# Kernel tuning notes

Measured on AMD Instinct MI355X. Metric: run time of the kernel, lower is better.

The kernel has to match this reference:

```python
import jax, jax.numpy as jnp
import numpy as np

B, N, F, D, H = 4, 2048, 128, 128, 4

def setup_inputs() -> dict:
    key = jax.random.key(0)
    k1, k2, k3, k4 = jax.random.split(key, 4)
    X = jax.random.normal(k1, (B, N, F), dtype=jnp.float32)
    A = jax.random.uniform(k2, (B, N, N), dtype=jnp.float32)
    kernel = jax.random.normal(k3, (F, D), dtype=jnp.float32) * 0.05
    bias = jnp.ones((D,), dtype=jnp.float32)
    attn = jax.random.normal(k4, (H, D, D), dtype=jnp.float32) * 0.05
    return {"X": X, "A": A, "kernel": kernel, "bias": bias, "attn": attn}

def reference(X, A, kernel, bias, attn):
    # Linear projection: [B,N,F] @ [F,D] + bias -> [B,N,D]
    Xp = jnp.einsum('bnf,fd->bnd', X, kernel) + bias
    # Per-head bilinear scores Xp @ attn_h @ Xp^T, batched over heads: [B,H,N,N]
    scores = jnp.einsum('bnd,hde,bme->bhnm', Xp, attn, Xp)
    # Adjacency mask + tanh (fused elementwise)
    Am = jnp.tanh(A[:, None, :, :] * scores)
    # Weighted aggregate per head: [B,H,N,N] @ [B,N,D] -> [B,H,N,D]
    heads = jnp.einsum('bhnm,bmd->bhnd', Am, Xp)
    # Mean over heads, relu
    Xh = jax.nn.relu(jnp.mean(heads, axis=1))
    # Skip connection (shapes match since F == D): relu(Xh + X)
    out = jax.nn.relu(Xh + X)
    return out
```

## Files before the change

### kernel.cpp

```cpp
#include <hip/hip_runtime.h>

#define NB 4
#define NN 2048
#define ND 128
#define NH 4

typedef short short8 __attribute__((ext_vector_type(8)));
typedef short short4v __attribute__((ext_vector_type(4)));
typedef float floatx4 __attribute__((ext_vector_type(4)));

__device__ __forceinline__ short f2bf(float f){
  unsigned u = __float_as_uint(f);
  u += 0x7FFFu + ((u >> 16) & 1u);
  return (short)(u >> 16);
}
__device__ __forceinline__ float bf2f(short s){
  unsigned u = ((unsigned)(unsigned short)s) << 16;
  return __uint_as_float(u);
}

__global__ void k0_transpose(const float* __restrict__ W, const float* __restrict__ attn,
                             short* __restrict__ WT, short* __restrict__ attnT){
  int mat = blockIdx.x;
  const float* src = (mat == 0) ? W : (attn + (mat - 1) * 16384);
  short* dst = (mat == 0) ? WT : (attnT + (mat - 1) * 16384);
  __shared__ short tile[128 * 130];
  int t = threadIdx.x;
  for (int k = 0; k < 64; ++k){
    int idx = k * 256 + t;
    int r = idx >> 7, c = idx & 127;
    tile[c * 130 + r] = f2bf(src[idx]);
  }
  __syncthreads();
  for (int k = 0; k < 8; ++k){
    int g = k * 256 + t;
    int r = g >> 4, c8 = g & 15;
    short8 v;
    #pragma unroll
    for (int j = 0; j < 8; ++j) v[j] = tile[r * 130 + c8 * 8 + j];
    *(short8*)&dst[r * 128 + c8 * 8] = v;
  }
}

__global__ __launch_bounds__(256) void k1_xp(const float* __restrict__ X,
                                             const short* __restrict__ WT,
                                             const float* __restrict__ bias,
                                             short* __restrict__ Xp){
  int bid = blockIdx.x;
  int b = bid >> 5, i0 = (bid & 31) << 6;
  int t = threadIdx.x, w = t >> 6, lane = t & 63, lq = lane >> 4, lc = lane & 15;
  __shared__ __align__(16) short ldsB[16384];
  #pragma unroll
  for (int c = 0; c < 8; ++c){
    int q = c * 256 + t; int fblk = q >> 7; int d = q & 127;
    *(short8*)&ldsB[q * 8] = *(const short8*)&WT[d * 128 + fblk * 8];
  }
  short8 af[4][4];
  #pragma unroll
  for (int ib = 0; ib < 4; ++ib)
    #pragma unroll
    for (int k = 0; k < 4; ++k){
      const float* xp = &X[(b * NN + i0 + ib * 16 + lc) * ND + k * 32 + lq * 8];
      float4 x0 = *(const float4*)xp;
      float4 x1 = *(const float4*)(xp + 4);
      short8 s;
      s[0]=f2bf(x0.x); s[1]=f2bf(x0.y); s[2]=f2bf(x0.z); s[3]=f2bf(x0.w);
      s[4]=f2bf(x1.x); s[5]=f2bf(x1.y); s[6]=f2bf(x1.z); s[7]=f2bf(x1.w);
      af[ib][k] = s;
    }
  __syncthreads();
  floatx4 acc[4][2];
  #pragma unroll
  for (int ib = 0; ib < 4; ++ib)
    #pragma unroll
    for (int eb = 0; eb < 2; ++eb) acc[ib][eb] = (floatx4){0.f, 0.f, 0.f, 0.f};
  #pragma unroll
  for (int eb = 0; eb < 2; ++eb)
    #pragma unroll
    for (int k = 0; k < 4; ++k){
      short8 bf = *(short8*)&ldsB[(k * 4 + lq) * 1024 + (w * 32 + eb * 16 + lc) * 8];
      #pragma unroll
      for (int ib = 0; ib < 4; ++ib)
        acc[ib][eb] = __builtin_amdgcn_mfma_f32_16x16x32_bf16(af[ib][k], bf, acc[ib][eb], 0, 0, 0);
    }
  #pragma unroll
  for (int ib = 0; ib < 4; ++ib)
    #pragma unroll
    for (int eb = 0; eb < 2; ++eb){
      int d = w * 32 + eb * 16 + lc;
      float bv = bias[d];
      #pragma unroll
      for (int r = 0; r < 4; ++r){
        int n = i0 + ib * 16 + lq * 4 + r;
        Xp[(b * NN + n) * ND + d] = f2bf(acc[ib][eb][r] + bv);
      }
    }
}

__global__ void k1b_transpose(const short* __restrict__ Xp, short* __restrict__ XpT){
  int bid = blockIdx.x;
  int b = bid >> 6; int rem = bid & 63;
  int n0 = (rem >> 1) << 6, d0 = (rem & 1) << 6;
  __shared__ short tile[64 * 66];
  int t = threadIdx.x;
  #pragma unroll
  for (int c = 0; c < 2; ++c){
    int g = c * 256 + t; int r = g >> 3, c8 = g & 7;
    short8 v = *(const short8*)&Xp[(b * NN + n0 + r) * ND + d0 + c8 * 8];
    #pragma unroll
    for (int j = 0; j < 8; ++j) tile[(c8 * 8 + j) * 66 + r] = v[j];
  }
  __syncthreads();
  #pragma unroll
  for (int c = 0; c < 2; ++c){
    int g = c * 256 + t; int d = g >> 3, n8 = g & 7;
    short8 v;
    #pragma unroll
    for (int j = 0; j < 8; ++j) v[j] = tile[d * 66 + n8 * 8 + j];
    *(short8*)&XpT[(b * ND + d0 + d) * NN + n0 + n8 * 8] = v;
  }
}

__global__ __launch_bounds__(256) void k2_y(const short* __restrict__ Xp,
                                            const short* __restrict__ attnT,
                                            short* __restrict__ Y){
  int bid = blockIdx.x;
  int it = bid & 31, h = (bid >> 5) & 3, b = bid >> 7;
  int i0 = it << 6;
  int t = threadIdx.x, w = t >> 6, lane = t & 63, lq = lane >> 4, lc = lane & 15;
  __shared__ __align__(16) short ldsB[16384];
  const short* Bsrc = attnT + h * 16384;
  #pragma unroll
  for (int c = 0; c < 8; ++c){
    int q = c * 256 + t; int dblk = q >> 7; int e = q & 127;
    *(short8*)&ldsB[q * 8] = *(const short8*)&Bsrc[e * 128 + dblk * 8];
  }
  short8 af[4][4];
  #pragma unroll
  for (int ib = 0; ib < 4; ++ib)
    #pragma unroll
    for (int k = 0; k < 4; ++k)
      af[ib][k] = *(const short8*)&Xp[(b * NN + i0 + ib * 16 + lc) * ND + k * 32 + lq * 8];
  __syncthreads();
  floatx4 acc[4][2];
  #pragma unroll
  for (int ib = 0; ib < 4; ++ib)
    #pragma unroll
    for (int eb = 0; eb < 2; ++eb) acc[ib][eb] = (floatx4){0.f, 0.f, 0.f, 0.f};
  #pragma unroll
  for (int eb = 0; eb < 2; ++eb)
    #pragma unroll
    for (int k = 0; k < 4; ++k){
      short8 bf = *(short8*)&ldsB[(k * 4 + lq) * 1024 + (w * 32 + eb * 16 + lc) * 8];
      #pragma unroll
      for (int ib = 0; ib < 4; ++ib)
        acc[ib][eb] = __builtin_amdgcn_mfma_f32_16x16x32_bf16(af[ib][k], bf, acc[ib][eb], 0, 0, 0);
    }
  #pragma unroll
  for (int ib = 0; ib < 4; ++ib)
    #pragma unroll
    for (int eb = 0; eb < 2; ++eb){
      int e = w * 32 + eb * 16 + lc;
      #pragma unroll
      for (int r = 0; r < 4; ++r){
        int n = i0 + ib * 16 + lq * 4 + r;
        Y[((b * NH + h) * NN + n) * ND + e] = f2bf(acc[ib][eb][r]);
      }
    }
}

__global__ __launch_bounds__(256, 3) void k3_fused(const short* __restrict__ Xp,
                                                   const short* __restrict__ XpT,
                                                   const short* __restrict__ Y,
                                                   const float* __restrict__ A,
                                                   float* __restrict__ part){
  int bid = blockIdx.x;
  int it = bid & 127, b = (bid >> 7) & 3, ms = bid >> 9;
  int i0 = it << 4;
  int t = threadIdx.x, w = t >> 6, lane = t & 63, lq = lane >> 4, lc = lane & 15;

  __shared__ __align__(16) short ldsXpT[2][8320];
  __shared__ __align__(16) short ldsPh[2][1024];
  __shared__ __align__(16) short ldsPl[2][1024];

  short8 yf[4][4];
  #pragma unroll
  for (int h = 0; h < 4; ++h)
    #pragma unroll
    for (int k = 0; k < 4; ++k)
      yf[h][k] = *(const short8*)&Y[((b * NH + h) * NN + i0 + lc) * ND + k * 32 + lq * 8];

  floatx4 acc[2];
  acc[0] = (floatx4){0.f,0.f,0.f,0.f};
  acc[1] = (floatx4){0.f,0.f,0.f,0.f};

  const int mbase = ms << 9;
  const int poff = (w * 2 + (lq >> 1)) * 128 + lc * 8 + (lq & 1) * 4;

  for (int itn = 0; itn < 8; ++itn){
    int p = itn & 1;
    int m0 = mbase + itn * 64;
    const short* src = XpT + b * (ND * NN) + m0;
    #pragma unroll
    for (int c = 0; c < 4; ++c){
      int q = c * 256 + t; int d = q >> 3, mb = q & 7;
      *(short8*)&ldsXpT[p][mb * 1040 + d * 8] = *(const short8*)&src[d * NN + mb * 8];
    }
    short8 xpf[4];
    const short* xr = Xp + (b * NN + m0 + w * 16 + lc) * ND;
    #pragma unroll
    for (int k = 0; k < 4; ++k) xpf[k] = *(const short8*)&xr[k * 32 + lq * 8];
    floatx4 av = *(const floatx4*)&A[(b * NN + i0 + lc) * NN + m0 + w * 16 + lq * 4];

    float psum[4] = {0.f, 0.f, 0.f, 0.f};
    #pragma unroll
    for (int h = 0; h < 4; ++h){
      floatx4 S = (floatx4){0.f,0.f,0.f,0.f};
      #pragma unroll
      for (int k = 0; k < 4; ++k)
        S = __builtin_amdgcn_mfma_f32_16x16x32_bf16(xpf[k], yf[h][k], S, 0, 0, 0);
      #pragma unroll
      for (int r = 0; r < 4; ++r){
        float x = av[r] * S[r];
        float e = __builtin_amdgcn_exp2f(x * 2.885390081777926f);
        psum[r] += 1.f - 2.f * __builtin_amdgcn_rcpf(e + 1.f);
      }
    }
    short4v hi4, lo4;
    #pragma unroll
    for (int r = 0; r < 4; ++r){
      float pb = 0.25f * psum[r];
      short h16 = f2bf(pb);
      hi4[r] = h16;
      lo4[r] = f2bf(pb - bf2f(h16));
    }
    *(short4v*)&ldsPh[p][poff] = hi4;
    *(short4v*)&ldsPl[p][poff] = lo4;
    __syncthreads();

    #pragma unroll
    for (int kb = 0; kb < 2; ++kb){
      short8 ph = *(short8*)&ldsPh[p][(kb * 4 + lq) * 128 + lc * 8];
      short8 pl = *(short8*)&ldsPl[p][(kb * 4 + lq) * 128 + lc * 8];
      #pragma unroll
      for (int db = 0; db < 2; ++db){
        short8 bfr = *(short8*)&ldsXpT[p][(kb * 4 + lq) * 1040 + (w * 32 + db * 16 + lc) * 8];
        acc[db] = __builtin_amdgcn_mfma_f32_16x16x32_bf16(ph, bfr, acc[db], 0, 0, 0);
        acc[db] = __builtin_amdgcn_mfma_f32_16x16x32_bf16(pl, bfr, acc[db], 0, 0, 0);
      }
    }
  }
  float* dst = part + (size_t)ms * 1048576 + (b * NN + i0) * ND;
  #pragma unroll
  for (int db = 0; db < 2; ++db)
    #pragma unroll
    for (int r = 0; r < 4; ++r)
      dst[(lq * 4 + r) * ND + w * 32 + db * 16 + lc] = acc[db][r];
}

__global__ void k4_final(const float* __restrict__ part, const float* __restrict__ X,
                         float* __restrict__ out){
  int f = (blockIdx.x * 256 + threadIdx.x) * 4;
  float4 s0 = *(const float4*)(part + f);
  float4 s1 = *(const float4*)(part + 1048576 + f);
  float4 s2 = *(const float4*)(part + 2097152 + f);
  float4 s3 = *(const float4*)(part + 3145728 + f);
  float4 xv = *(const float4*)(X + f);
  float4 o;
  o.x = fmaxf(fmaxf(s0.x + s1.x + s2.x + s3.x, 0.f) + xv.x, 0.f);
  o.y = fmaxf(fmaxf(s0.y + s1.y + s2.y + s3.y, 0.f) + xv.y, 0.f);
  o.z = fmaxf(fmaxf(s0.z + s1.z + s2.z + s3.z, 0.f) + xv.z, 0.f);
  o.w = fmaxf(fmaxf(s0.w + s1.w + s2.w + s3.w, 0.f) + xv.w, 0.f);
  *(float4*)(out + f) = o;
}

extern "C" void kernel_launch(void* const* d_in, const int* in_sizes, int n_in,
                              void* d_out, int out_size, void* d_ws, size_t ws_size,
                              hipStream_t stream) {
  const float* X    = (const float*)d_in[0];
  const float* A    = (const float*)d_in[1];
  const float* W    = (const float*)d_in[2];
  const float* bias = (const float*)d_in[3];
  const float* attn = (const float*)d_in[4];
  float* out = (float*)d_out;

  const size_t OFF_XP    = 0;
  const size_t OFF_XPT   = (size_t)2 << 20;
  const size_t OFF_Y     = (size_t)4 << 20;
  const size_t OFF_PART  = (size_t)12 << 20;
  const size_t OFF_WT    = (size_t)28 << 20;
  const size_t OFF_ATTNT = OFF_WT + 32768;
  const size_t NEED = OFF_ATTNT + 131072;
  if (ws_size < NEED) return;

  char* ws = (char*)d_ws;
  short* Xp    = (short*)(ws + OFF_XP);
  short* XpT   = (short*)(ws + OFF_XPT);
  short* Y     = (short*)(ws + OFF_Y);
  float* part  = (float*)(ws + OFF_PART);
  short* WT    = (short*)(ws + OFF_WT);
  short* attnT = (short*)(ws + OFF_ATTNT);

  k0_transpose<<<5, 256, 0, stream>>>(W, attn, WT, attnT);
  k1_xp<<<128, 256, 0, stream>>>(X, WT, bias, Xp);
  k1b_transpose<<<256, 256, 0, stream>>>(Xp, XpT);
  k2_y<<<512, 256, 0, stream>>>(Xp, attnT, Y);
  k3_fused<<<2048, 256, 0, stream>>>(Xp, XpT, Y, A, part);
  k4_final<<<1024, 256, 0, stream>>>(part, X, out);
}
```

Before: 190.9 us.

## Fold weight transposes and Xp transpose into projection kernels, drop two launches

The weight and attention matrix bf16 transposes move out of a separate kernel: each block now converts and scatters them straight into LDS in the packed layout the MFMA loop reads. The Xp transpose kernel is merged into k1_xp, which stages its output tile in LDS and writes XpT directly. This cuts the pipeline from six launches to four and removes an intermediate round trip. In exchange, every k2 block repeats the fp32 load and conversion of a full attention matrix with scalar LDS stores, adding per-block work.

```diff
diff --git a/kernel.cpp b/kernel.cpp
--- a/kernel.cpp
+++ b/kernel.cpp
@@ -19,41 +19,18 @@
   return __uint_as_float(u);
 }
 
-__global__ void k0_transpose(const float* __restrict__ W, const float* __restrict__ attn,
-                             short* __restrict__ WT, short* __restrict__ attnT){
-  int mat = blockIdx.x;
-  const float* src = (mat == 0) ? W : (attn + (mat - 1) * 16384);
-  short* dst = (mat == 0) ? WT : (attnT + (mat - 1) * 16384);
-  __shared__ short tile[128 * 130];
-  int t = threadIdx.x;
-  for (int k = 0; k < 64; ++k){
-    int idx = k * 256 + t;
-    int r = idx >> 7, c = idx & 127;
-    tile[c * 130 + r] = f2bf(src[idx]);
-  }
-  __syncthreads();
-  for (int k = 0; k < 8; ++k){
-    int g = k * 256 + t;
-    int r = g >> 4, c8 = g & 15;
-    short8 v;
-    #pragma unroll
-    for (int j = 0; j < 8; ++j) v[j] = tile[r * 130 + c8 * 8 + j];
-    *(short8*)&dst[r * 128 + c8 * 8] = v;
-  }
-}
-
 __global__ __launch_bounds__(256) void k1_xp(const float* __restrict__ X,
-                                             const short* __restrict__ WT,
+                                             const float* __restrict__ W,
                                              const float* __restrict__ bias,
-                                             short* __restrict__ Xp){
+                                             short* __restrict__ Xp,
+                                             short* __restrict__ XpT){
   int bid = blockIdx.x;
   int b = bid >> 5, i0 = (bid & 31) << 6;
   int t = threadIdx.x, w = t >> 6, lane = t & 63, lq = lane >> 4, lc = lane & 15;
   __shared__ __align__(16) short ldsB[16384];
-  #pragma unroll
-  for (int c = 0; c < 8; ++c){
-    int q = c * 256 + t; int fblk = q >> 7; int d = q & 127;
-    *(short8*)&ldsB[q * 8] = *(const short8*)&WT[d * 128 + fblk * 8];
+  for (int k = 0; k < 64; ++k){
+    int idx = k * 256 + t; int f = idx >> 7, d = idx & 127;
+    ldsB[((f >> 3) * 128 + d) * 8 + (f & 7)] = f2bf(W[idx]);
   }
   short8 af[4][4];
   #pragma unroll
@@ -83,6 +60,8 @@
       for (int ib = 0; ib < 4; ++ib)
         acc[ib][eb] = __builtin_amdgcn_mfma_f32_16x16x32_bf16(af[ib][k], bf, acc[ib][eb], 0, 0, 0);
     }
+  __syncthreads();
+  short* tr = ldsB;
   #pragma unroll
   for (int ib = 0; ib < 4; ++ib)
     #pragma unroll
@@ -92,48 +71,34 @@
       #pragma unroll
       for (int r = 0; r < 4; ++r){
         int n = i0 + ib * 16 + lq * 4 + r;
-        Xp[(b * NN + n) * ND + d] = f2bf(acc[ib][eb][r] + bv);
-      }
-    }
-}
-
-__global__ void k1b_transpose(const short* __restrict__ Xp, short* __restrict__ XpT){
-  int bid = blockIdx.x;
-  int b = bid >> 6; int rem = bid & 63;
-  int n0 = (rem >> 1) << 6, d0 = (rem & 1) << 6;
-  __shared__ short tile[64 * 66];
-  int t = threadIdx.x;
-  #pragma unroll
-  for (int c = 0; c < 2; ++c){
-    int g = c * 256 + t; int r = g >> 3, c8 = g & 7;
-    short8 v = *(const short8*)&Xp[(b * NN + n0 + r) * ND + d0 + c8 * 8];
-    #pragma unroll
-    for (int j = 0; j < 8; ++j) tile[(c8 * 8 + j) * 66 + r] = v[j];
-  }
-  __syncthreads();
-  #pragma unroll
-  for (int c = 0; c < 2; ++c){
+        short s = f2bf(acc[ib][eb][r] + bv);
+        Xp[(b * NN + n) * ND + d] = s;
+        tr[d * 72 + (n - i0)] = s;
+      }
+    }
+  __syncthreads();
+  #pragma unroll
+  for (int c = 0; c < 4; ++c){
     int g = c * 256 + t; int d = g >> 3, n8 = g & 7;
     short8 v;
     #pragma unroll
-    for (int j = 0; j < 8; ++j) v[j] = tile[d * 66 + n8 * 8 + j];
-    *(short8*)&XpT[(b * ND + d0 + d) * NN + n0 + n8 * 8] = v;
+    for (int j = 0; j < 8; ++j) v[j] = tr[d * 72 + n8 * 8 + j];
+    *(short8*)&XpT[(b * ND + d) * NN + i0 + n8 * 8] = v;
   }
 }
 
 __global__ __launch_bounds__(256) void k2_y(const short* __restrict__ Xp,
-                                            const short* __restrict__ attnT,
+                                            const float* __restrict__ attn,
                                             short* __restrict__ Y){
   int bid = blockIdx.x;
   int it = bid & 31, h = (bid >> 5) & 3, b = bid >> 7;
   int i0 = it << 6;
   int t = threadIdx.x, w = t >> 6, lane = t & 63, lq = lane >> 4, lc = lane & 15;
   __shared__ __align__(16) short ldsB[16384];
-  const short* Bsrc = attnT + h * 16384;
-  #pragma unroll
-  for (int c = 0; c < 8; ++c){
-    int q = c * 256 + t; int dblk = q >> 7; int e = q & 127;
-    *(short8*)&ldsB[q * 8] = *(const short8*)&Bsrc[e * 128 + dblk * 8];
+  const float* Asrc = attn + h * 16384;
+  for (int k = 0; k < 64; ++k){
+    int idx = k * 256 + t; int dd = idx >> 7, e = idx & 127;
+    ldsB[((dd >> 3) * 128 + e) * 8 + (dd & 7)] = f2bf(Asrc[idx]);
   }
   short8 af[4][4];
   #pragma unroll
@@ -288,9 +253,7 @@
   const size_t OFF_XPT   = (size_t)2 << 20;
   const size_t OFF_Y     = (size_t)4 << 20;
   const size_t OFF_PART  = (size_t)12 << 20;
-  const size_t OFF_WT    = (size_t)28 << 20;
-  const size_t OFF_ATTNT = OFF_WT + 32768;
-  const size_t NEED = OFF_ATTNT + 131072;
+  const size_t NEED = (size_t)28 << 20;
   if (ws_size < NEED) return;
 
   char* ws = (char*)d_ws;
@@ -298,13 +261,9 @@
   short* XpT   = (short*)(ws + OFF_XPT);
   short* Y     = (short*)(ws + OFF_Y);
   float* part  = (float*)(ws + OFF_PART);
-  short* WT    = (short*)(ws + OFF_WT);
-  short* attnT = (short*)(ws + OFF_ATTNT);
-
-  k0_transpose<<<5, 256, 0, stream>>>(W, attn, WT, attnT);
-  k1_xp<<<128, 256, 0, stream>>>(X, WT, bias, Xp);
-  k1b_transpose<<<256, 256, 0, stream>>>(Xp, XpT);
-  k2_y<<<512, 256, 0, stream>>>(Xp, attnT, Y);
+
+  k1_xp<<<128, 256, 0, stream>>>(X, W, bias, Xp, XpT);
+  k2_y<<<512, 256, 0, stream>>>(Xp, attn, Y);
   k3_fused<<<2048, 256, 0, stream>>>(Xp, XpT, Y, A, part);
   k4_final<<<1024, 256, 0, stream>>>(part, X, out);
 }
```

New measurement: 186.6 us. -2.3%, faster.
